# Optimization experiments

Measured on AMD Instinct MI355X. Metric: run time of the kernel, lower is better.

The kernel has to match this reference:

```python
import jax, jax.numpy as jnp
import numpy as np
import math

D_MODEL = 1024
N_HEAD = 16
NEG = -1e10  # matches torch masked_fill value

def setup_inputs() -> dict:
    key = jax.random.key(0)
    ks = jax.random.split(key, 5)
    B, S, D = 2, 2048, D_MODEL
    s = 0.02
    return {
        "x": jax.random.normal(ks[0], (B, S, D), jnp.float32),
        "w_qkv": jax.random.normal(ks[1], (3 * D, D), jnp.float32) * s,  # torch Linear weight [out,in]
        "b_qkv": jnp.zeros((3 * D,), jnp.float32),
        "w_out": jax.random.normal(ks[2], (D, D), jnp.float32) * s,
        "b_out": jnp.zeros((D,), jnp.float32),
    }

def reference(x, w_qkv, b_qkv, w_out, b_out):
    B, S, D = x.shape
    H = N_HEAD
    dk = D // H
    qkv = x @ w_qkv.T + b_qkv                      # [B,S,3D]
    q, k, v = jnp.split(qkv, 3, axis=2)
    def heads(t):
        return t.reshape(B, S, H, dk).transpose(0, 2, 1, 3)  # [B,H,S,dk]
    q, k, v = heads(q), heads(k), heads(v)
    scores = jnp.einsum('bhqd,bhkd->bhqk', q, k) / math.sqrt(dk)
    mask = jnp.tril(jnp.ones((S, S), bool))
    scores = jnp.where(mask, scores, NEG)
    attn = jax.nn.softmax(scores, axis=-1)
    out = jnp.einsum('bhqk,bhkd->bhqd', attn, v)   # [B,H,S,dk]
    out = out.transpose(0, 2, 1, 3).reshape(B, S, D)
    return out @ w_out.T + b_out
```

## Files before the change

### kernel.cpp

```cpp
#include <hip/hip_runtime.h>

typedef __attribute__((ext_vector_type(8))) short short8;
typedef __attribute__((ext_vector_type(4))) float floatx4;

#define DMODEL 1024
#define NHEAD  16
#define DK     64
#define SEQ    2048
#define QSCALE 0.18033688011112042f

__device__ __forceinline__ unsigned short f2bf(float f) {
  unsigned u = __builtin_bit_cast(unsigned, f);
  u += 0x7FFF + ((u >> 16) & 1);
  return (unsigned short)(u >> 16);
}

__global__ void f2bf_all(const float* __restrict__ x, const float* __restrict__ wq,
                         const float* __restrict__ wo,
                         unsigned short* __restrict__ xb, unsigned short* __restrict__ wqb,
                         unsigned short* __restrict__ wob) {
  const int n1 = 1048576;
  const int n2 = 786432;
  const int n3 = 262144;
  int i = blockIdx.x * 256 + threadIdx.x;
  int stride = gridDim.x * 256;
  for (; i < n1 + n2 + n3; i += stride) {
    const float* src; unsigned short* dst; int j;
    if (i < n1)            { src = x;  dst = xb;  j = i; }
    else if (i < n1 + n2)  { src = wq; dst = wqb; j = i - n1; }
    else                   { src = wo; dst = wob; j = i - n1 - n2; }
    float4 v = reinterpret_cast<const float4*>(src)[j];
    ushort4 o;
    o.x = f2bf(v.x); o.y = f2bf(v.y); o.z = f2bf(v.z); o.w = f2bf(v.w);
    reinterpret_cast<ushort4*>(dst)[j] = o;
  }
}

__device__ __forceinline__ void gload16(const void* g, void* l) {
  __builtin_amdgcn_global_load_lds((const __attribute__((address_space(1))) void*)g,
                                   (__attribute__((address_space(3))) void*)l, 16, 0, 0);
}

__global__ __launch_bounds__(256)
void gemm_qkv(const unsigned short* __restrict__ A, const unsigned short* __restrict__ Bt,
              const float* __restrict__ bias,
              unsigned short* __restrict__ Qo, unsigned short* __restrict__ Ko,
              unsigned short* __restrict__ Vro) {
  const int K = DMODEL;
  __shared__ short Al[2][128 * 32];
  __shared__ short Bl[2][128 * 32];
  const int tid = threadIdx.x, lane = tid & 63, wave = tid >> 6;
  const int wr = wave >> 1, wc = wave & 1;
  const int m0 = blockIdx.x * 128, n0 = blockIdx.y * 128;

  floatx4 z4 = {0.f, 0.f, 0.f, 0.f};
  floatx4 acc[4][4];
#pragma unroll
  for (int i = 0; i < 4; i++)
#pragma unroll
    for (int j = 0; j < 4; j++) acc[i][j] = z4;

  auto STAGE = [&](int sb, int k0) {
#pragma unroll
    for (int i = 0; i < 2; i++) {
      int chunk = wave * 2 + i;
      int e = chunk * 512 + lane * 8;
      int row = e >> 5, kc = e & 31;
      gload16(A  + (size_t)(m0 + row) * K + k0 + kc, &Al[sb][chunk * 512]);
      gload16(Bt + (size_t)(n0 + row) * K + k0 + kc, &Bl[sb][chunk * 512]);
    }
  };

  STAGE(0, 0);
  int buf = 0;
  for (int k0 = 0; k0 < K; k0 += 32) {
    __syncthreads();
    if (k0 + 32 < K) STAGE(buf ^ 1, k0 + 32);
    const short* Ac = Al[buf];
    const short* Bc = Bl[buf];
    short8 af[4], bfr[4];
#pragma unroll
    for (int i = 0; i < 4; i++) {
      af[i]  = *reinterpret_cast<const short8*>(&Ac[(wr * 64 + i * 16 + (lane & 15)) * 32 + ((lane >> 4) << 3)]);
      bfr[i] = *reinterpret_cast<const short8*>(&Bc[(wc * 64 + i * 16 + (lane & 15)) * 32 + ((lane >> 4) << 3)]);
    }
#pragma unroll
    for (int i = 0; i < 4; i++)
#pragma unroll
      for (int j = 0; j < 4; j++)
        acc[i][j] = __builtin_amdgcn_mfma_f32_16x16x32_bf16(af[i], bfr[j], acc[i][j], 0, 0, 0);
    buf ^= 1;
  }

#pragma unroll
  for (int i = 0; i < 4; i++) {
#pragma unroll
    for (int j = 0; j < 4; j++) {
#pragma unroll
      for (int r = 0; r < 4; r++) {
        int m = m0 + wr * 64 + i * 16 + ((lane >> 4) << 2) + r;
        int n = n0 + wc * 64 + j * 16 + (lane & 15);
        float v = acc[i][j][r] + bias[n];
        int which = n >> 10;
        int h = (n & 1023) >> 6;
        int d = n & 63;
        int b = m >> 11, s = m & 2047;
        int bh = (b << 4) + h;
        size_t idx = ((size_t)bh * SEQ + s) * DK + d;
        if (which == 0)      Qo[idx]  = f2bf(v * QSCALE);
        else if (which == 1) Ko[idx]  = f2bf(v);
        else                 Vro[idx] = f2bf(v);
      }
    }
  }
}

__global__ __launch_bounds__(256)
void transpose_v(const unsigned short* __restrict__ Vr, unsigned short* __restrict__ Vt) {
  __shared__ unsigned short T[64][68];
  const int tid = threadIdx.x;
  const int bh = blockIdx.x, st = blockIdx.y;
  const int s0 = st * 64;
  const unsigned short* src = Vr + ((size_t)bh * SEQ + s0) * DK;
#pragma unroll
  for (int i = 0; i < 4; i++) {
    int idx = tid + 256 * i;
    int row = idx >> 4, c = (idx & 15) << 2;
    ushort4 v = *reinterpret_cast<const ushort4*>(&src[row * DK + c]);
    *reinterpret_cast<ushort4*>(&T[row][c]) = v;
  }
  __syncthreads();
  unsigned short* dst = Vt + (size_t)bh * DK * SEQ + s0;
#pragma unroll
  for (int i = 0; i < 4; i++) {
    int idx = tid + 256 * i;
    int d = idx >> 4, sc = (idx & 15) << 2;
    ushort4 o;
    o.x = T[sc + 0][d]; o.y = T[sc + 1][d]; o.z = T[sc + 2][d]; o.w = T[sc + 3][d];
    *reinterpret_cast<ushort4*>(&dst[(size_t)d * SEQ + sc]) = o;
  }
}

__global__ __launch_bounds__(256)
void attn_kernel(const unsigned short* __restrict__ Qb, const unsigned short* __restrict__ Kb,
                 const unsigned short* __restrict__ Vtb, unsigned short* __restrict__ AO)
{
  __shared__ short Kl[2][4096];
  __shared__ short Vl[2][4096];
  __shared__ short Pl[4][1024];
  const int tid = threadIdx.x, lane = tid & 63, wave = tid >> 6;
  const int bh = blockIdx.x, y = blockIdx.y;
  const int b = bh >> 4, h = bh & 15;
  const unsigned short* Qh = Qb  + (size_t)bh * SEQ * DK;
  const unsigned short* Kh = Kb  + (size_t)bh * SEQ * DK;
  const unsigned short* Vh = Vtb + (size_t)bh * DK * SEQ;
  short* Pw = Pl[wave];
  const int lrb = (lane >> 4) << 2;

  floatx4 z4 = {0.f, 0.f, 0.f, 0.f};
  const floatx4 minit = {-8.f, -8.f, -8.f, -8.f};

  const int srow = lane >> 3;
  const int srk  = ((lane & 7) ^ srow) << 3;
  auto STAGE = [&](int sb, int kv0) {
#pragma unroll
    for (int sub = 0; sub < 2; sub++) {
      int row = wave * 16 + sub * 8 + srow;
      gload16(Kh + (size_t)(kv0 + row) * DK + srk, &Kl[sb][wave * 1024 + sub * 512]);
      gload16(Vh + (size_t)row * SEQ + kv0 + srk,  &Vl[sb][wave * 1024 + sub * 512]);
    }
  };

#pragma unroll
  for (int ph = 0; ph < 2; ph++) {
    const int qt = (ph == 0) ? y : (31 - y);
    const int q0 = qt * 64;
    const int qrow_w = q0 + wave * 16;

    short8 qf[2];
    {
      int arow = qrow_w + (lane & 15);
#pragma unroll
      for (int ks = 0; ks < 2; ks++)
        qf[ks] = *reinterpret_cast<const short8*>(&Qh[(size_t)arow * DK + ks * 32 + ((lane >> 4) << 3)]);
    }

    floatx4 o[4];
    float lsum[4] = {0.f, 0.f, 0.f, 0.f};
#pragma unroll
    for (int db = 0; db < 4; db++) o[db] = z4;

    if (ph == 1) __syncthreads();
    const int ntiles = qt + 1;
    STAGE(0, 0);
    int buf = 0;
    for (int it = 0; it < ntiles; it++) {
      __syncthreads();
      if (it + 1 < ntiles) STAGE(buf ^ 1, (it + 1) * 64);
      const short* Kc = Kl[buf];
      const short* Vc = Vl[buf];
      buf ^= 1;
      const int kv0 = it * 64;

      floatx4 sc[4];
#pragma unroll
      for (int nb = 0; nb < 4; nb++) sc[nb] = minit;
#pragma unroll
      for (int ks = 0; ks < 2; ks++) {
#pragma unroll
        for (int nb = 0; nb < 4; nb++) {
          int kvr = nb * 16 + (lane & 15);
          short8 kf = *reinterpret_cast<const short8*>(
              &Kc[((kvr << 6) + ks * 32 + ((lane >> 4) << 3)) ^ ((kvr & 7) << 3)]);
          sc[nb] = __builtin_amdgcn_mfma_f32_16x16x32_bf16(qf[ks], kf, sc[nb], 0, 0, 0);
        }
      }

      if (it == ntiles - 1) {
        int kvb = kv0 + (lane & 15);
        int qr = qrow_w + lrb;
#pragma unroll
        for (int nb = 0; nb < 4; nb++)
#pragma unroll
          for (int r = 0; r < 4; r++)
            sc[nb][r] = (kvb + nb * 16 <= qr + r) ? sc[nb][r] : -1e30f;
      }

#pragma unroll
      for (int nb = 0; nb < 4; nb++)
#pragma unroll
        for (int r = 0; r < 4; r++) {
          float p = __builtin_amdgcn_exp2f(sc[nb][r]);
          lsum[r] += p;
          int lr = lrb + r;
          Pw[((lr << 6) + nb * 16 + (lane & 15)) ^ ((lr & 7) << 3)] =
              (short)(__builtin_bit_cast(unsigned, p) >> 16);
        }

#pragma unroll
      for (int ks2 = 0; ks2 < 2; ks2++) {
        int lr = lane & 15;
        short8 pf = *reinterpret_cast<const short8*>(
            &Pw[((lr << 6) + ks2 * 32 + ((lane >> 4) << 3)) ^ ((lr & 7) << 3)]);
#pragma unroll
        for (int db = 0; db < 4; db++) {
          int dr = db * 16 + (lane & 15);
          short8 vf = *reinterpret_cast<const short8*>(
              &Vc[((dr << 6) + ks2 * 32 + ((lane >> 4) << 3)) ^ ((dr & 7) << 3)]);
          o[db] = __builtin_amdgcn_mfma_f32_16x16x32_bf16(pf, vf, o[db], 0, 0, 0);
        }
      }
    }

#pragma unroll
    for (int msk = 1; msk < 16; msk <<= 1)
#pragma unroll
      for (int r = 0; r < 4; r++) lsum[r] += __shfl_xor(lsum[r], msk);
    float rl[4];
#pragma unroll
    for (int r = 0; r < 4; r++) rl[r] = __builtin_amdgcn_rcpf(lsum[r]);

#pragma unroll
    for (int db = 0; db < 4; db++) {
#pragma unroll
      for (int r = 0; r < 4; r++) {
        int q = qrow_w + lrb + r;
        int d = db * 16 + (lane & 15);
        AO[((size_t)(b * SEQ + q)) * DMODEL + h * DK + d] = f2bf(o[db][r] * rl[r]);
      }
    }
  }
}

__global__ __launch_bounds__(256)
void gemm_out(const unsigned short* __restrict__ A, const unsigned short* __restrict__ Bt,
              const float* __restrict__ bias, float* __restrict__ Cf) {
  const int K = DMODEL, N = DMODEL;
  __shared__ short Al[2][64 * 32];
  __shared__ short Bl[2][128 * 32];
  const int tid = threadIdx.x, lane = tid & 63, wave = tid >> 6;
  const int wr = wave >> 1, wc = wave & 1;
  const int m0 = blockIdx.x * 64, n0 = blockIdx.y * 128;

  floatx4 z4 = {0.f, 0.f, 0.f, 0.f};
  floatx4 acc[2][4];
#pragma unroll
  for (int i = 0; i < 2; i++)
#pragma unroll
    for (int j = 0; j < 4; j++) acc[i][j] = z4;

  auto STAGE = [&](int sb, int k0) {
    {
      int e = wave * 512 + lane * 8;
      int row = e >> 5, kc = e & 31;
      gload16(A + (size_t)(m0 + row) * K + k0 + kc, &Al[sb][wave * 512]);
    }
#pragma unroll
    for (int i = 0; i < 2; i++) {
      int chunk = wave * 2 + i;
      int e = chunk * 512 + lane * 8;
      int row = e >> 5, kc = e & 31;
      gload16(Bt + (size_t)(n0 + row) * K + k0 + kc, &Bl[sb][chunk * 512]);
    }
  };

  STAGE(0, 0);
  int buf = 0;
  for (int k0 = 0; k0 < K; k0 += 32) {
    __syncthreads();
    if (k0 + 32 < K) STAGE(buf ^ 1, k0 + 32);
    const short* Ac = Al[buf];
    const short* Bc = Bl[buf];
    short8 af[2], bfr[4];
#pragma unroll
    for (int i = 0; i < 2; i++)
      af[i]  = *reinterpret_cast<const short8*>(&Ac[(wr * 32 + i * 16 + (lane & 15)) * 32 + ((lane >> 4) << 3)]);
#pragma unroll
    for (int j = 0; j < 4; j++)
      bfr[j] = *reinterpret_cast<const short8*>(&Bc[(wc * 64 + j * 16 + (lane & 15)) * 32 + ((lane >> 4) << 3)]);
#pragma unroll
    for (int i = 0; i < 2; i++)
#pragma unroll
      for (int j = 0; j < 4; j++)
        acc[i][j] = __builtin_amdgcn_mfma_f32_16x16x32_bf16(af[i], bfr[j], acc[i][j], 0, 0, 0);
    buf ^= 1;
  }

#pragma unroll
  for (int i = 0; i < 2; i++)
#pragma unroll
    for (int j = 0; j < 4; j++)
#pragma unroll
      for (int r = 0; r < 4; r++) {
        int m = m0 + wr * 32 + i * 16 + ((lane >> 4) << 2) + r;
        int n = n0 + wc * 64 + j * 16 + (lane & 15);
        Cf[(size_t)m * N + n] = acc[i][j][r] + bias[n];
      }
}

extern "C" void kernel_launch(void* const* d_in, const int* in_sizes, int n_in,
                              void* d_out, int out_size, void* d_ws, size_t ws_size,
                              hipStream_t stream) {
  (void)in_sizes; (void)n_in; (void)out_size; (void)ws_size;
  const float* x     = (const float*)d_in[0];
  const float* w_qkv = (const float*)d_in[1];
  const float* b_qkv = (const float*)d_in[2];
  const float* w_out = (const float*)d_in[3];
  const float* b_out = (const float*)d_in[4];
  float* out = (float*)d_out;

  char* ws = (char*)d_ws;
  unsigned short* xb    = (unsigned short*)(ws);
  unsigned short* wqkvb = (unsigned short*)(ws + (8u  << 20));
  unsigned short* woutb = (unsigned short*)(ws + (14u << 20));
  unsigned short* Qb    = (unsigned short*)(ws + (16u << 20));
  unsigned short* Kb    = (unsigned short*)(ws + (24u << 20));
  unsigned short* Vrow  = (unsigned short*)(ws + (32u << 20));
  unsigned short* Vtb   = (unsigned short*)(ws + (40u << 20));
  unsigned short* AOb   = xb;

  f2bf_all<<<2048, 256, 0, stream>>>(x, w_qkv, w_out, xb, wqkvb, woutb);

  gemm_qkv<<<dim3(32, 24), 256, 0, stream>>>(xb, wqkvb, b_qkv, Qb, Kb, Vrow);

  transpose_v<<<dim3(32, 32), 256, 0, stream>>>(Vrow, Vtb);

  attn_kernel<<<dim3(32, 16), 256, 0, stream>>>(Qb, Kb, Vtb, AOb);

  gemm_out<<<dim3(64, 8), 256, 0, stream>>>(AOb, woutb, b_out, out);
}
```

Before: 186.9 us.

## Fuse V transpose into QKV GEMM epilogue and swizzle GEMM LDS tiles

The QKV GEMM now writes V directly in transposed [bh, d, s] layout. It stages each 64-row half of the tile through LDS and stores along the sequence dimension, which removes the separate transpose_v kernel launch and its extra global round trip of V. Both GEMMs also apply an XOR swizzle to the LDS tile layout on the global-to-LDS loads and the fragment reads, meant to reduce LDS bank conflicts. The V-column blocks pay for this with extra syncthreads in the epilogue.

```diff
diff --git a/kernel.cpp b/kernel.cpp
--- a/kernel.cpp
+++ b/kernel.cpp
@@ -41,17 +41,20 @@
                                    (__attribute__((address_space(3))) void*)l, 16, 0, 0);
 }
 
+
 __global__ __launch_bounds__(256)
 void gemm_qkv(const unsigned short* __restrict__ A, const unsigned short* __restrict__ Bt,
               const float* __restrict__ bias,
               unsigned short* __restrict__ Qo, unsigned short* __restrict__ Ko,
-              unsigned short* __restrict__ Vro) {
+              unsigned short* __restrict__ Vto) {
   const int K = DMODEL;
-  __shared__ short Al[2][128 * 32];
-  __shared__ short Bl[2][128 * 32];
+  __shared__ short smem[4][4096];
   const int tid = threadIdx.x, lane = tid & 63, wave = tid >> 6;
   const int wr = wave >> 1, wc = wave & 1;
+  const int lrb = (lane >> 4) << 2;
   const int m0 = blockIdx.x * 128, n0 = blockIdx.y * 128;
+  const int sw_st = ((lane & 3) ^ ((lane >> 3) & 3)) << 3;
+  const int sw_rd = ((lane >> 4) ^ ((lane >> 1) & 3)) << 3;
 
   floatx4 z4 = {0.f, 0.f, 0.f, 0.f};
   floatx4 acc[4][4];
@@ -64,10 +67,9 @@
 #pragma unroll
     for (int i = 0; i < 2; i++) {
       int chunk = wave * 2 + i;
-      int e = chunk * 512 + lane * 8;
-      int row = e >> 5, kc = e & 31;
-      gload16(A  + (size_t)(m0 + row) * K + k0 + kc, &Al[sb][chunk * 512]);
-      gload16(Bt + (size_t)(n0 + row) * K + k0 + kc, &Bl[sb][chunk * 512]);
+      int row = chunk * 16 + (lane >> 2);
+      gload16(A  + (size_t)(m0 + row) * K + k0 + sw_st, &smem[sb][chunk * 512]);
+      gload16(Bt + (size_t)(n0 + row) * K + k0 + sw_st, &smem[2 + sb][chunk * 512]);
     }
   };
 
@@ -76,13 +78,13 @@
   for (int k0 = 0; k0 < K; k0 += 32) {
     __syncthreads();
     if (k0 + 32 < K) STAGE(buf ^ 1, k0 + 32);
-    const short* Ac = Al[buf];
-    const short* Bc = Bl[buf];
+    const short* Ac = smem[buf];
+    const short* Bc = smem[2 + buf];
     short8 af[4], bfr[4];
 #pragma unroll
     for (int i = 0; i < 4; i++) {
-      af[i]  = *reinterpret_cast<const short8*>(&Ac[(wr * 64 + i * 16 + (lane & 15)) * 32 + ((lane >> 4) << 3)]);
-      bfr[i] = *reinterpret_cast<const short8*>(&Bc[(wc * 64 + i * 16 + (lane & 15)) * 32 + ((lane >> 4) << 3)]);
+      af[i]  = *reinterpret_cast<const short8*>(&Ac[(wr * 64 + i * 16 + (lane & 15)) * 32 + sw_rd]);
+      bfr[i] = *reinterpret_cast<const short8*>(&Bc[(wc * 64 + i * 16 + (lane & 15)) * 32 + sw_rd]);
     }
 #pragma unroll
     for (int i = 0; i < 4; i++)
@@ -92,52 +94,58 @@
     buf ^= 1;
   }
 
-#pragma unroll
-  for (int i = 0; i < 4; i++) {
-#pragma unroll
-    for (int j = 0; j < 4; j++) {
-#pragma unroll
-      for (int r = 0; r < 4; r++) {
-        int m = m0 + wr * 64 + i * 16 + ((lane >> 4) << 2) + r;
-        int n = n0 + wc * 64 + j * 16 + (lane & 15);
-        float v = acc[i][j][r] + bias[n];
-        int which = n >> 10;
-        int h = (n & 1023) >> 6;
-        int d = n & 63;
-        int b = m >> 11, s = m & 2047;
-        int bh = (b << 4) + h;
-        size_t idx = ((size_t)bh * SEQ + s) * DK + d;
-        if (which == 0)      Qo[idx]  = f2bf(v * QSCALE);
-        else if (which == 1) Ko[idx]  = f2bf(v);
-        else                 Vro[idx] = f2bf(v);
-      }
-    }
-  }
-}
-
-__global__ __launch_bounds__(256)
-void transpose_v(const unsigned short* __restrict__ Vr, unsigned short* __restrict__ Vt) {
-  __shared__ unsigned short T[64][68];
-  const int tid = threadIdx.x;
-  const int bh = blockIdx.x, st = blockIdx.y;
-  const int s0 = st * 64;
-  const unsigned short* src = Vr + ((size_t)bh * SEQ + s0) * DK;
-#pragma unroll
-  for (int i = 0; i < 4; i++) {
-    int idx = tid + 256 * i;
-    int row = idx >> 4, c = (idx & 15) << 2;
-    ushort4 v = *reinterpret_cast<const ushort4*>(&src[row * DK + c]);
-    *reinterpret_cast<ushort4*>(&T[row][c]) = v;
-  }
-  __syncthreads();
-  unsigned short* dst = Vt + (size_t)bh * DK * SEQ + s0;
-#pragma unroll
-  for (int i = 0; i < 4; i++) {
-    int idx = tid + 256 * i;
-    int d = idx >> 4, sc = (idx & 15) << 2;
-    ushort4 o;
-    o.x = T[sc + 0][d]; o.y = T[sc + 1][d]; o.z = T[sc + 2][d]; o.w = T[sc + 3][d];
-    *reinterpret_cast<ushort4*>(&dst[(size_t)d * SEQ + sc]) = o;
+  if (n0 < 2048) {
+#pragma unroll
+    for (int i = 0; i < 4; i++) {
+#pragma unroll
+      for (int j = 0; j < 4; j++) {
+#pragma unroll
+        for (int r = 0; r < 4; r++) {
+          int m = m0 + wr * 64 + i * 16 + lrb + r;
+          int n = n0 + wc * 64 + j * 16 + (lane & 15);
+          float v = acc[i][j][r] + bias[n];
+          int h = (n & 1023) >> 6;
+          int d = n & 63;
+          int b = m >> 11, s = m & 2047;
+          size_t idx = ((size_t)((b << 4) + h) * SEQ + s) * DK + d;
+          if ((n >> 10) == 0) Qo[idx] = f2bf(v * QSCALE);
+          else                Ko[idx] = f2bf(v);
+        }
+      }
+    }
+  } else {
+    const int h0 = (n0 - 2048) >> 6;
+    const int b = m0 >> 11;
+    const int s0 = m0 & 2047;
+    short (*Vlds)[72] = (short (*)[72])smem;
+#pragma unroll
+    for (int p = 0; p < 2; p++) {
+      __syncthreads();
+      if (wr == p) {
+#pragma unroll
+        for (int i = 0; i < 4; i++)
+#pragma unroll
+          for (int j = 0; j < 4; j++)
+#pragma unroll
+            for (int r = 0; r < 4; r++) {
+              int nl = wc * 64 + j * 16 + (lane & 15);
+              float v = acc[i][j][r] + bias[n0 + nl];
+              Vlds[nl][i * 16 + lrb + r] = (short)f2bf(v);
+            }
+      }
+      __syncthreads();
+#pragma unroll
+      for (int k = 0; k < 8; k++) {
+        int idx = tid + 256 * k;
+        int row = idx >> 4;
+        int c4 = (idx & 15) << 2;
+        int h = h0 + (row >> 6);
+        int d = row & 63;
+        ushort4 vv = *reinterpret_cast<const ushort4*>(&Vlds[row][c4]);
+        *reinterpret_cast<ushort4*>(
+            &Vto[((size_t)(((b << 4) + h) * DK + d)) * SEQ + s0 + p * 64 + c4]) = vv;
+      }
+    }
   }
 }
 
@@ -281,6 +289,8 @@
   const int tid = threadIdx.x, lane = tid & 63, wave = tid >> 6;
   const int wr = wave >> 1, wc = wave & 1;
   const int m0 = blockIdx.x * 64, n0 = blockIdx.y * 128;
+  const int sw_st = ((lane & 3) ^ ((lane >> 3) & 3)) << 3;
+  const int sw_rd = ((lane >> 4) ^ ((lane >> 1) & 3)) << 3;
 
   floatx4 z4 = {0.f, 0.f, 0.f, 0.f};
   floatx4 acc[2][4];
@@ -291,16 +301,14 @@
 
   auto STAGE = [&](int sb, int k0) {
     {
-      int e = wave * 512 + lane * 8;
-      int row = e >> 5, kc = e & 31;
-      gload16(A + (size_t)(m0 + row) * K + k0 + kc, &Al[sb][wave * 512]);
+      int row = wave * 16 + (lane >> 2);
+      gload16(A + (size_t)(m0 + row) * K + k0 + sw_st, &Al[sb][wave * 512]);
     }
 #pragma unroll
     for (int i = 0; i < 2; i++) {
       int chunk = wave * 2 + i;
-      int e = chunk * 512 + lane * 8;
-      int row = e >> 5, kc = e & 31;
-      gload16(Bt + (size_t)(n0 + row) * K + k0 + kc, &Bl[sb][chunk * 512]);
+      int row = chunk * 16 + (lane >> 2);
+      gload16(Bt + (size_t)(n0 + row) * K + k0 + sw_st, &Bl[sb][chunk * 512]);
     }
   };
 
@@ -314,10 +322,10 @@
     short8 af[2], bfr[4];
 #pragma unroll
     for (int i = 0; i < 2; i++)
-      af[i]  = *reinterpret_cast<const short8*>(&Ac[(wr * 32 + i * 16 + (lane & 15)) * 32 + ((lane >> 4) << 3)]);
+      af[i]  = *reinterpret_cast<const short8*>(&Ac[(wr * 32 + i * 16 + (lane & 15)) * 32 + sw_rd]);
 #pragma unroll
     for (int j = 0; j < 4; j++)
-      bfr[j] = *reinterpret_cast<const short8*>(&Bc[(wc * 64 + j * 16 + (lane & 15)) * 32 + ((lane >> 4) << 3)]);
+      bfr[j] = *reinterpret_cast<const short8*>(&Bc[(wc * 64 + j * 16 + (lane & 15)) * 32 + sw_rd]);
 #pragma unroll
     for (int i = 0; i < 2; i++)
 #pragma unroll
@@ -355,15 +363,12 @@
   unsigned short* woutb = (unsigned short*)(ws + (14u << 20));
   unsigned short* Qb    = (unsigned short*)(ws + (16u << 20));
   unsigned short* Kb    = (unsigned short*)(ws + (24u << 20));
-  unsigned short* Vrow  = (unsigned short*)(ws + (32u << 20));
-  unsigned short* Vtb   = (unsigned short*)(ws + (40u << 20));
+  unsigned short* Vtb   = (unsigned short*)(ws + (32u << 20));
   unsigned short* AOb   = xb;
 
   f2bf_all<<<2048, 256, 0, stream>>>(x, w_qkv, w_out, xb, wqkvb, woutb);
 
-  gemm_qkv<<<dim3(32, 24), 256, 0, stream>>>(xb, wqkvb, b_qkv, Qb, Kb, Vrow);
-
-  transpose_v<<<dim3(32, 32), 256, 0, stream>>>(Vrow, Vtb);
+  gemm_qkv<<<dim3(32, 24), 256, 0, stream>>>(xb, wqkvb, b_qkv, Qb, Kb, Vtb);
 
   attn_kernel<<<dim3(32, 16), 256, 0, stream>>>(Qb, Kb, Vtb, AOb);
 
```

Result: faster. 182.8 us (-2.1%).
